# Kernel optimization log

Hardware: AMD Instinct MI355X
Metric: run time of the kernel (lower is better)

Reference implementation:

```python
import jax, jax.numpy as jnp
import numpy as np

B, S, D_IN, D_OUT = 4, 2048, 1024, 1024


def setup_inputs() -> dict:
    key = jax.random.key(0)
    k1, k2, k3, k4 = jax.random.split(key, 4)
    scale = 1.0 / np.sqrt(D_IN)
    return {
        "x": jax.random.normal(k1, (B, S, D_IN), dtype=jnp.float32),
        "W_q": jax.random.normal(k2, (D_OUT, D_IN), dtype=jnp.float32) * scale,
        "W_k": jax.random.normal(k3, (D_OUT, D_IN), dtype=jnp.float32) * scale,
        "W_v": jax.random.normal(k4, (D_OUT, D_IN), dtype=jnp.float32) * scale,
    }


def reference(x, W_q, W_k, W_v):
    # torch nn.Linear: y = x @ W.T (bias=False)
    q = jnp.einsum("bsd,od->bso", x, W_q)
    k = jnp.einsum("bsd,od->bso", x, W_k)
    v = jnp.einsum("bsd,od->bso", x, W_v)
    s = q.shape[1]
    scores = jnp.einsum("bqo,bko->bqk", q, k)  # [B, S, S]
    causal = jnp.triu(jnp.ones((s, s), dtype=bool), k=1)
    scores = jnp.where(causal, -jnp.inf, scores)
    inv_sqrt_d = 1.0 / jnp.sqrt(jnp.asarray(q.shape[-1], scores.dtype))
    attn = jax.nn.softmax(scores * inv_sqrt_d, axis=-1)
    # dropout p=0.0 -> identity (deterministic reference)
    return jnp.einsum("bqk,bko->bqo", attn, v)
```

## Files before the change

kernel.cpp:

```cpp
#include <hip/hip_runtime.h>

typedef unsigned short u16;
typedef __bf16 bf16x8 __attribute__((ext_vector_type(8)));
typedef float f32x4 __attribute__((ext_vector_type(4)));

#define AS1 __attribute__((address_space(1)))
#define AS3 __attribute__((address_space(3)))

__device__ inline u16 f2bf(float f) {
  union { float f; unsigned u; } a; a.f = f;
  unsigned u = a.u;
  return (u16)((u + 0x7fffu + ((u >> 16) & 1u)) >> 16);
}

__global__ __launch_bounds__(256) void cvt_all_kernel(
    const float* __restrict__ x, const float* __restrict__ wq,
    const float* __restrict__ wk, const float* __restrict__ wv,
    u16* __restrict__ xb, u16* __restrict__ wqb,
    u16* __restrict__ wkb, u16* __restrict__ wvb) {
  int bid = blockIdx.x;
  const float* in; u16* out;
  if (bid < 8192) { in = x; out = xb; }
  else if (bid < 9216) { in = wq; out = wqb; bid -= 8192; }
  else if (bid < 10240) { in = wk; out = wkb; bid -= 9216; }
  else { in = wv; out = wvb; bid -= 10240; }
  size_t i = ((size_t)bid * 256 + threadIdx.x) * 4;
  float4 v = *(const float4*)(in + i);
  ushort4 o;
  o.x = f2bf(v.x); o.y = f2bf(v.y); o.z = f2bf(v.z); o.w = f2bf(v.w);
  *(ushort4*)(out + i) = o;
}

template <typename CT, int BN>
__device__ __forceinline__ void gemm_core(
    u16* __restrict__ lds,
    const u16* __restrict__ A, const u16* __restrict__ B, CT* __restrict__ C,
    int nt, int lda, int ldb, int ldc, int m0, int n0) {
  constexpr int ABUF = 16384;
  constexpr int BBUF = BN * 64;
  constexpr int BSW = BN / 64;
  constexpr int NI = BN / 64;

  const int tid = threadIdx.x;
  const int ln = tid & 63, wv = tid >> 6;
  const int wr = wv >> 2, wc = wv & 3;

  auto sweep = [&](const u16* src, int ld, int t, int s, int base) {
    const int c = s * 512 + tid;
    const int row = c >> 3, slot = c & 7;
    const int col = (slot ^ (row & 7)) * 8;
    __builtin_amdgcn_global_load_lds(
        (const AS1 void*)(src + (size_t)row * ld + (size_t)t * 64 + col),
        (AS3 void*)(&lds[base + c * 8]), 16, 0, 0);
  };

  f32x4 acc[8][NI] = {};

#pragma unroll
  for (int s = 0; s < BSW; ++s) sweep(B, ldb, 0, s, 2 * ABUF);
#pragma unroll
  for (int s = 0; s < 4; ++s) sweep(A, lda, 0, s, 0);
  if (nt > 1) {
#pragma unroll
    for (int s = 0; s < BSW; ++s) sweep(B, ldb, 1, s, 2 * ABUF + BBUF);
#pragma unroll
    for (int s = 0; s < 4; ++s) sweep(A, lda, 1, s, ABUF);
    if constexpr (BSW == 4) asm volatile("s_waitcnt vmcnt(8)" ::: "memory");
    else                    asm volatile("s_waitcnt vmcnt(6)" ::: "memory");
  } else {
    asm volatile("s_waitcnt vmcnt(0)" ::: "memory");
  }
  __builtin_amdgcn_s_barrier();

  for (int t = 0; t < nt; ++t) {
    const int p = t & 1;
    const u16* La = &lds[p * ABUF];
    const u16* Lb = &lds[2 * ABUF + p * BBUF];
    bf16x8 bfr[NI][2];
#pragma unroll
    for (int q = 0; q < 4; ++q) {
      if (q == 0) {
        __builtin_amdgcn_sched_barrier(0);
#pragma unroll
        for (int ni = 0; ni < NI; ++ni)
#pragma unroll
          for (int ks = 0; ks < 2; ++ks) {
            const int row = wc * (BN / 4) + ni * 16 + (ln & 15);
            const int kc = ks * 4 + (ln >> 4);
            bfr[ni][ks] = *(const bf16x8*)&Lb[row * 64 + ((kc ^ (row & 7)) << 3)];
          }
      }
      bf16x8 afr[2][2];
#pragma unroll
      for (int mi = 0; mi < 2; ++mi)
#pragma unroll
        for (int ks = 0; ks < 2; ++ks) {
          const int row = wr * 128 + (q * 2 + mi) * 16 + (ln & 15);
          const int kc = ks * 4 + (ln >> 4);
          afr[mi][ks] = *(const bf16x8*)&La[row * 64 + ((kc ^ (row & 7)) << 3)];
        }
      if (q == 0)      { if (t >= 1 && t + 1 < nt) { sweep(A, lda, t + 1, 0, (p ^ 1) * ABUF); sweep(A, lda, t + 1, 1, (p ^ 1) * ABUF); } }
      else if (q == 1) { if (t >= 1 && t + 1 < nt) { sweep(A, lda, t + 1, 2, (p ^ 1) * ABUF); sweep(A, lda, t + 1, 3, (p ^ 1) * ABUF); } }
      else if (q == 2) { if (t + 2 < nt) { sweep(B, ldb, t + 2, 0, 2 * ABUF + p * BBUF); if (BSW == 4) sweep(B, ldb, t + 2, 1, 2 * ABUF + p * BBUF); } }
      else             { if (t + 2 < nt) { if (BSW == 4) { sweep(B, ldb, t + 2, 2, 2 * ABUF + p * BBUF); sweep(B, ldb, t + 2, 3, 2 * ABUF + p * BBUF); } else { sweep(B, ldb, t + 2, 1, 2 * ABUF + p * BBUF); } } }

      __builtin_amdgcn_s_barrier();
      __builtin_amdgcn_s_setprio(1);
#pragma unroll
      for (int mi = 0; mi < 2; ++mi)
#pragma unroll
        for (int ni = 0; ni < NI; ++ni)
#pragma unroll
          for (int ks = 0; ks < 2; ++ks)
            acc[q * 2 + mi][ni] = __builtin_amdgcn_mfma_f32_16x16x32_bf16(
                afr[mi][ks], bfr[ni][ks], acc[q * 2 + mi][ni], 0, 0, 0);
      __builtin_amdgcn_s_setprio(0);
      if (q == 3) {
        if (t + 2 < nt) {
          if constexpr (BSW == 4) asm volatile("s_waitcnt vmcnt(4)" ::: "memory");
          else                    asm volatile("s_waitcnt vmcnt(2)" ::: "memory");
        } else if (t + 1 < nt) {
          asm volatile("s_waitcnt vmcnt(0)" ::: "memory");
        }
      }
      __builtin_amdgcn_s_barrier();
    }
  }

#pragma unroll
  for (int mi = 0; mi < 8; ++mi) {
    const int rbase = m0 + wr * 128 + mi * 16 + (ln >> 4) * 4;
#pragma unroll
    for (int ni = 0; ni < NI; ++ni) {
      const int col = n0 + wc * (BN / 4) + ni * 16 + (ln & 15);
#pragma unroll
      for (int r = 0; r < 4; ++r) {
        const float v = acc[mi][ni][r];
        CT* ptr = &C[(size_t)(rbase + r) * ldc + col];
        if constexpr (sizeof(CT) == 4) *(float*)ptr = v;
        else                           *ptr = f2bf(v);
      }
    }
  }
}

__global__ __launch_bounds__(512, 2) void proj_qk_kernel(
    const u16* __restrict__ xb, const u16* __restrict__ wqb,
    const u16* __restrict__ wkb, u16* __restrict__ Qb, u16* __restrict__ Kb) {
  __shared__ __align__(16) u16 lds[65536];
  const int bid = blockIdx.x;
  const int w = bid >> 7, r = bid & 127;
  const int rb = r >> 2, n0 = (r & 3) * 256;
  const u16* B = w ? wkb : wqb;
  u16* C = w ? Kb : Qb;
  gemm_core<u16, 256>(lds, xb + (size_t)rb * 256 * 1024, B + (size_t)n0 * 1024,
                      C, 16, 1024, 1024, 1024, rb * 256, n0);
}

__global__ __launch_bounds__(512, 2) void vtqkt2_kernel(
    const u16* __restrict__ Qb, const u16* __restrict__ Kb, float* __restrict__ Sb,
    const u16* __restrict__ wvb, const u16* __restrict__ xb, u16* __restrict__ VTb) {
  __shared__ __align__(16) u16 lds[65536];
  const int bid = blockIdx.x;
  if (bid < 32) {
    const int z = bid >> 3, m = (bid >> 1) & 3, n = bid & 1;
    gemm_core<u16, 256>(lds, wvb + (size_t)m * 256 * 1024,
                        xb + (size_t)z * 2048 * 1024 + (size_t)n * 256 * 1024,
                        VTb + (size_t)z * 1024 * 2048,
                        16, 1024, 1024, 2048, m * 256, n * 256);
  } else if (bid < 320) {
    const int j = bid - 32;
    const int z = j / 72, r = j % 72;
    int m = 0;
    while ((m + 1) * (m + 2) <= r) ++m;
    const int h = r - m * (m + 1);
    gemm_core<float, 128>(lds,
        Qb + ((size_t)z * 2048 + m * 256) * 1024,
        Kb + ((size_t)z * 2048 + h * 128) * 1024,
        Sb + (size_t)z * 2048 * 2048,
        16, 1024, 1024, 2048, m * 256, h * 128);
  } else {
    const int j = bid - 320;
    const int z = j >> 5, r = j & 31;
    const int m = r >> 3, nf = r & 7;
    const int n0 = 512 + nf * 128;
    gemm_core<u16, 128>(lds, wvb + (size_t)m * 256 * 1024,
                        xb + (size_t)z * 2048 * 1024 + (size_t)n0 * 1024,
                        VTb + (size_t)z * 1024 * 2048,
                        16, 1024, 1024, 2048, m * 256, n0);
  }
}

__global__ __launch_bounds__(512, 2) void smvt_kernel(
    float* __restrict__ Sb,
    const u16* __restrict__ wvb, const u16* __restrict__ xb, u16* __restrict__ VTb) {
  __shared__ __align__(16) u16 lds[65536];
  const int bid = blockIdx.x;
  const int tid = threadIdx.x;
  if (bid < 64) {
    const int z = bid >> 4, r = bid & 15;
    const int m = r >> 2, nf = 8 + (r & 3);
    const int n0 = 512 + nf * 128;
    gemm_core<u16, 128>(lds, wvb + (size_t)m * 256 * 1024,
                        xb + (size_t)z * 2048 * 1024 + (size_t)n0 * 1024,
                        VTb + (size_t)z * 1024 * 2048,
                        16, 1024, 1024, 2048, m * 256, n0);
    return;
  }
  const int j = bid - 64;
  const int m = 7 - (j >> 6), z = (j >> 4) & 3, s = j & 15;
  const int iters = m + 1;
  const int wvid = tid >> 6, lane = tid & 63;
  float* S0 = Sb + (size_t)z * 2048 * 2048;
  for (int rr = wvid; rr < 16; rr += 8) {
    const int r = m * 256 + s * 16 + rr;
    float* row = S0 + (size_t)r * 2048;
    float vals[8][4];
    float mx = -3.4e38f;
#pragma unroll
    for (int it2 = 0; it2 < 8; ++it2)
      if (it2 < iters) {
        const int idx = it2 * 64 + lane;
        float4 v = ((const float4*)row)[idx];
        const int j0 = idx * 4;
        vals[it2][0] = (j0 <= r) ? v.x * 0.03125f : -3.4e38f;
        vals[it2][1] = (j0 + 1 <= r) ? v.y * 0.03125f : -3.4e38f;
        vals[it2][2] = (j0 + 2 <= r) ? v.z * 0.03125f : -3.4e38f;
        vals[it2][3] = (j0 + 3 <= r) ? v.w * 0.03125f : -3.4e38f;
        mx = fmaxf(mx, fmaxf(fmaxf(vals[it2][0], vals[it2][1]),
                             fmaxf(vals[it2][2], vals[it2][3])));
      }
#pragma unroll
    for (int o = 32; o; o >>= 1) mx = fmaxf(mx, __shfl_xor(mx, o, 64));
    float sum = 0.f;
#pragma unroll
    for (int it2 = 0; it2 < 8; ++it2)
      if (it2 < iters) {
#pragma unroll
        for (int e = 0; e < 4; ++e) {
          const float pp = __expf(vals[it2][e] - mx);
          vals[it2][e] = pp;
          sum += pp;
        }
      }
#pragma unroll
    for (int o = 32; o; o >>= 1) sum += __shfl_xor(sum, o, 64);
    const float rcp = 1.f / sum;
    u16* prow = (u16*)row;
#pragma unroll
    for (int it2 = 0; it2 < 8; ++it2)
      if (it2 < iters) {
        ushort4 o4;
        o4.x = f2bf(vals[it2][0] * rcp);
        o4.y = f2bf(vals[it2][1] * rcp);
        o4.z = f2bf(vals[it2][2] * rcp);
        o4.w = f2bf(vals[it2][3] * rcp);
        ((ushort4*)prow)[it2 * 64 + lane] = o4;
      }
  }
}

__constant__ signed char CPM[16] = {5,5,7,7,7,6,4,4,6,6,3,3,1,2,2,0};
__constant__ signed char CPK[16] = {0,12,0,11,22,0,0,10,10,19,0,8,0,0,6,0};
__constant__ signed char CPN[16] = {12,12,11,11,10,10,10,10,9,9,8,8,8,6,6,4};
__constant__ signed char CPS[16] = {0,1,0,1,2,0,0,1,1,2,0,1,0,0,1,0};

__global__ __launch_bounds__(512, 2) void pv_kernel(
    const u16* __restrict__ P, const u16* __restrict__ VTb,
    float* __restrict__ out, float* __restrict__ Sb) {
  __shared__ __align__(16) u16 lds[65536];
  const int cls = blockIdx.x, n = blockIdx.y;
  const size_t z = blockIdx.z;
  const int m = CPM[cls], k0 = CPK[cls], ntc = CPN[cls], sl = CPS[cls];
  const u16* Ap = P + z * 2048 * 4096 + (size_t)m * 256 * 4096 + (size_t)k0 * 64;
  const u16* Bp = VTb + z * 1024 * 2048 + (size_t)n * 256 * 2048 + (size_t)k0 * 64;
  float* Cp;
  int ldc;
  if (sl == 0) { Cp = out + z * 2048 * 1024; ldc = 1024; }
  else if (sl == 1) { Cp = Sb + z * 2048 * 2048 + 1024; ldc = 2048; }
  else { Cp = Sb + z * 2048 * 2048 + 1024 - (size_t)1536 * 2048; ldc = 2048; }
  gemm_core<float, 256>(lds, Ap, Bp, Cp, ntc, 4096, 2048, ldc, m * 256, n * 256);
}

__global__ __launch_bounds__(256) void reduce_kernel(float* __restrict__ out,
                                                     const float* __restrict__ Sb) {
  const int j = blockIdx.x;
  const int m = 2 + (j >> 5), z = (j >> 3) & 3, s = j & 7;
  float* ob = out + (size_t)z * 2048 * 1024;
  const float* s1 = Sb + (size_t)z * 2048 * 2048 + 1024;
  const float* s2 = s1 - (size_t)1536 * 2048;
  const int r0 = m * 256 + s * 32;
  for (int k = threadIdx.x; k < 32 * 256; k += 256) {
    const int rr = r0 + (k >> 8), cc = k & 255;
    float4 o = ((float4*)(ob + (size_t)rr * 1024))[cc];
    float4 a = ((const float4*)(s1 + (size_t)rr * 2048))[cc];
    o.x += a.x; o.y += a.y; o.z += a.z; o.w += a.w;
    if (m >= 6) {
      float4 b = ((const float4*)(s2 + (size_t)rr * 2048))[cc];
      o.x += b.x; o.y += b.y; o.z += b.z; o.w += b.w;
    }
    ((float4*)(ob + (size_t)rr * 1024))[cc] = o;
  }
}

extern "C" void kernel_launch(void* const* d_in, const int* in_sizes, int n_in,
                              void* d_out, int out_size, void* d_ws, size_t ws_size,
                              hipStream_t stream) {
  const float* x  = (const float*)d_in[0];
  const float* Wq = (const float*)d_in[1];
  const float* Wk = (const float*)d_in[2];
  const float* Wv = (const float*)d_in[3];
  float* out = (float*)d_out;

  char* ws = (char*)d_ws;
  u16* xb   = (u16*)(ws);
  u16* wqb  = (u16*)(ws + (16ul << 20));
  u16* wkb  = (u16*)(ws + (18ul << 20));
  u16* wvb  = (u16*)(ws + (20ul << 20));
  u16* Qb   = (u16*)(ws + (22ul << 20));
  u16* Kb   = (u16*)(ws + (38ul << 20));
  u16* VTb  = (u16*)(ws + (54ul << 20));
  float* Sb = (float*)(ws + (70ul << 20));

  cvt_all_kernel<<<11264, 256, 0, stream>>>(x, Wq, Wk, Wv, xb, wqb, wkb, wvb);

  proj_qk_kernel<<<256, 512, 0, stream>>>(xb, wqb, wkb, Qb, Kb);

  vtqkt2_kernel<<<448, 512, 0, stream>>>(Qb, Kb, Sb, wvb, xb, VTb);

  smvt_kernel<<<576, 512, 0, stream>>>(Sb, wvb, xb, VTb);

  pv_kernel<<<dim3(16, 4, 4), 512, 0, stream>>>((const u16*)Sb, VTb, out, Sb);

  reduce_kernel<<<192, 256, 0, stream>>>(out, Sb);
}
```

Measured before the change: 165.2 us.

## Rebalance QK^T and V^T tiling, split last V^T column block with split-K

Replaces the mixed 256/128-tile QK^T and V^T scheduling with uniform 256x256 tiles: 144 causal QK^T tiles plus 112 V^T tiles covering the first seven 256-column blocks. The last V^T column block is computed in the softmax kernel as split-K partials written into unused fp32 scratch in the score buffer, then summed and converted to bf16 by a new small fixup kernel. The aim is fewer, larger tiles and better work balance across the kernel boundaries. It adds an extra launch and relies on that scratch region of the score buffer being free while the softmax rows are written.

```diff
diff --git a/kernel.cpp b/kernel.cpp
--- a/kernel.cpp
+++ b/kernel.cpp
@@ -157,54 +157,47 @@
                       C, 16, 1024, 1024, 1024, rb * 256, n0);
 }
 
-__global__ __launch_bounds__(512, 2) void vtqkt2_kernel(
+__global__ __launch_bounds__(512, 2) void qktvt_kernel(
     const u16* __restrict__ Qb, const u16* __restrict__ Kb, float* __restrict__ Sb,
     const u16* __restrict__ wvb, const u16* __restrict__ xb, u16* __restrict__ VTb) {
   __shared__ __align__(16) u16 lds[65536];
   const int bid = blockIdx.x;
-  if (bid < 32) {
-    const int z = bid >> 3, m = (bid >> 1) & 3, n = bid & 1;
-    gemm_core<u16, 256>(lds, wvb + (size_t)m * 256 * 1024,
-                        xb + (size_t)z * 2048 * 1024 + (size_t)n * 256 * 1024,
+  if (bid < 144) {
+    const int z = bid / 36, xt = bid % 36;
+    int m = 0;
+    while ((m + 1) * (m + 2) / 2 <= xt) ++m;
+    const int n = xt - m * (m + 1) / 2;
+    gemm_core<float, 256>(lds,
+        Qb + ((size_t)z * 2048 + m * 256) * 1024,
+        Kb + ((size_t)z * 2048 + n * 256) * 1024,
+        Sb + (size_t)z * 2048 * 2048,
+        16, 1024, 1024, 2048, m * 256, n * 256);
+  } else {
+    const int j = bid - 144;
+    const int z = j / 28, r2 = j % 28, d = r2 / 7, kb = r2 % 7;
+    gemm_core<u16, 256>(lds, wvb + (size_t)d * 256 * 1024,
+                        xb + (size_t)z * 2048 * 1024 + (size_t)kb * 256 * 1024,
                         VTb + (size_t)z * 1024 * 2048,
-                        16, 1024, 1024, 2048, m * 256, n * 256);
-  } else if (bid < 320) {
-    const int j = bid - 32;
-    const int z = j / 72, r = j % 72;
-    int m = 0;
-    while ((m + 1) * (m + 2) <= r) ++m;
-    const int h = r - m * (m + 1);
-    gemm_core<float, 128>(lds,
-        Qb + ((size_t)z * 2048 + m * 256) * 1024,
-        Kb + ((size_t)z * 2048 + h * 128) * 1024,
-        Sb + (size_t)z * 2048 * 2048,
-        16, 1024, 1024, 2048, m * 256, h * 128);
-  } else {
-    const int j = bid - 320;
-    const int z = j >> 5, r = j & 31;
-    const int m = r >> 3, nf = r & 7;
-    const int n0 = 512 + nf * 128;
-    gemm_core<u16, 128>(lds, wvb + (size_t)m * 256 * 1024,
-                        xb + (size_t)z * 2048 * 1024 + (size_t)n0 * 1024,
-                        VTb + (size_t)z * 1024 * 2048,
-                        16, 1024, 1024, 2048, m * 256, n0);
-  }
-}
-
-__global__ __launch_bounds__(512, 2) void smvt_kernel(
+                        16, 1024, 1024, 2048, d * 256, kb * 256);
+  }
+}
+
+__global__ __launch_bounds__(512, 2) void smvtk_kernel(
     float* __restrict__ Sb,
-    const u16* __restrict__ wvb, const u16* __restrict__ xb, u16* __restrict__ VTb) {
+    const u16* __restrict__ wvb, const u16* __restrict__ xb) {
   __shared__ __align__(16) u16 lds[65536];
   const int bid = blockIdx.x;
   const int tid = threadIdx.x;
   if (bid < 64) {
     const int z = bid >> 4, r = bid & 15;
-    const int m = r >> 2, nf = 8 + (r & 3);
-    const int n0 = 512 + nf * 128;
-    gemm_core<u16, 128>(lds, wvb + (size_t)m * 256 * 1024,
-                        xb + (size_t)z * 2048 * 1024 + (size_t)n0 * 1024,
-                        VTb + (size_t)z * 1024 * 2048,
-                        16, 1024, 1024, 2048, m * 256, n0);
+    const int d = r >> 2, kf = (r >> 1) & 1, h = r & 1;
+    const u16* A = wvb + (size_t)d * 256 * 1024 + h * 512;
+    const u16* B = xb + ((size_t)z * 2048 + 1792 + kf * 128) * 1024 + h * 512;
+    const int i = (d * 2 + kf) * 2 + h;
+    const int band = i >> 3, coli = i & 7;
+    float* C = Sb + (size_t)z * 2048 * 2048 + (size_t)band * 256 * 2048 +
+               1024 + coli * 128;
+    gemm_core<float, 128>(lds, A, B, C, 8, 1024, 1024, 2048, 0, 0);
     return;
   }
   const int j = bid - 64;
@@ -257,6 +250,29 @@
         o4.w = f2bf(vals[it2][3] * rcp);
         ((ushort4*)prow)[it2 * 64 + lane] = o4;
       }
+  }
+}
+
+__global__ __launch_bounds__(256) void vtfix_kernel(const float* __restrict__ Sb,
+                                                    u16* __restrict__ VTb) {
+  const int bid = blockIdx.x;
+  const int z = bid >> 3, sdk = bid & 7;
+  const int d = sdk >> 1, kf = sdk & 1;
+  const int i0 = sdk * 2;
+  const int band = i0 >> 3, coli = i0 & 7;
+  const float* P0 = Sb + (size_t)z * 2048 * 2048 + (size_t)band * 256 * 2048 +
+                    1024 + coli * 128;
+  const float* P1 = P0 + 128;
+  u16* dst = VTb + (size_t)z * 1024 * 2048 + (size_t)d * 256 * 2048 +
+             1792 + kf * 128;
+  for (int k = threadIdx.x; k < 8192; k += 256) {
+    const int r = k >> 5, c4 = (k & 31) << 2;
+    float4 a = *(const float4*)(P0 + (size_t)r * 2048 + c4);
+    float4 b = *(const float4*)(P1 + (size_t)r * 2048 + c4);
+    ushort4 o;
+    o.x = f2bf(a.x + b.x); o.y = f2bf(a.y + b.y);
+    o.z = f2bf(a.z + b.z); o.w = f2bf(a.w + b.w);
+    *(ushort4*)(dst + (size_t)r * 2048 + c4) = o;
   }
 }
 
@@ -326,9 +342,11 @@
 
   proj_qk_kernel<<<256, 512, 0, stream>>>(xb, wqb, wkb, Qb, Kb);
 
-  vtqkt2_kernel<<<448, 512, 0, stream>>>(Qb, Kb, Sb, wvb, xb, VTb);
-
-  smvt_kernel<<<576, 512, 0, stream>>>(Sb, wvb, xb, VTb);
+  qktvt_kernel<<<256, 512, 0, stream>>>(Qb, Kb, Sb, wvb, xb, VTb);
+
+  smvtk_kernel<<<576, 512, 0, stream>>>(Sb, wvb, xb);
+
+  vtfix_kernel<<<32, 256, 0, stream>>>(Sb, VTb);
 
   pv_kernel<<<dim3(16, 4, 4), 512, 0, stream>>>((const u16*)Sb, VTb, out, Sb);
 
```

After: 172.7 us. 1.05x slower.
